# Optimization experiments

Hardware: AMD Instinct MI355X
Metric: run time of the kernel (lower is better)

## Reference

```python
import jax, jax.numpy as jnp
import numpy as np

B, S, I, E, D = 64, 512, 64, 256, 256  # batch, src_len, input_size, enc_hid, dec_hid


def _lstm_cell(h, c, x, Wih, Whh, b):
    # PyTorch LSTM gate order: i, f, g, o ; b = b_ih + b_hh combined
    z = x @ Wih.T + h @ Whh.T + b
    i, f, g, o = jnp.split(z, 4, axis=-1)
    c = jax.nn.sigmoid(f) * c + jax.nn.sigmoid(i) * jnp.tanh(g)
    h = jax.nn.sigmoid(o) * jnp.tanh(c)
    return h, c


def _run_lstm(x, h0, c0, Wih, Whh, b):
    # x: [B,S,I] -> outputs [B,S,H]
    def step(carry, xt):
        h, c = _lstm_cell(carry[0], carry[1], xt, Wih, Whh, b)
        return (h, c), h
    _, ys = jax.lax.scan(step, (h0, c0), jnp.swapaxes(x, 0, 1))
    return jnp.swapaxes(ys, 0, 1)


def _forward(x, enc_h0, enc_c0, dec_h0, dec_c0, Wih_f, Whh_f, b_f, Wih_b, Whh_b, b_b,
             W_attn, b_attn, v, Wih_d, Whh_d, b_d, W_lin, b_lin):
    b_, s_ = x.shape[0], x.shape[1]
    # bidirectional encoder
    out_f = _run_lstm(x, enc_h0[0], enc_c0[0], Wih_f, Whh_f, b_f)
    out_b = _run_lstm(x[:, ::-1, :], enc_h0[1], enc_c0[1], Wih_b, Whh_b, b_b)[:, ::-1, :]
    enc_out = jnp.concatenate([out_f, out_b], axis=-1)  # [B,S,2E]
    h0d, c0d = dec_h0[0], dec_c0[0]  # decoder re-starts from these EVERY step (faithful)

    @jax.checkpoint
    def dec_step(carry, _):
        y, h_attn = carry  # y: [B,1], h_attn: [B,D]
        dh = h_attn.shape[-1]
        cat = jnp.concatenate(
            [jnp.broadcast_to(h_attn[:, None, :], (b_, s_, dh)), enc_out], axis=-1)
        energy = jnp.tanh(cat @ W_attn.T + b_attn)              # [B,S,D]
        attn = jax.nn.softmax(jnp.einsum('d,bsd->bs', v, energy), axis=1)
        context = jnp.einsum('bs,bse->be', attn, enc_out)       # [B,2E]
        dec_in = jnp.concatenate([y, context], axis=-1)         # [B,1+2E]
        h_new, _c = _lstm_cell(h0d, c0d, dec_in, Wih_d, Whh_d, b_d)
        y_new = jnp.concatenate([h_new, context], axis=-1) @ W_lin.T + b_lin  # [B,1]
        return (y_new, h_new), y_new

    y0 = jnp.zeros((b_, 1), dtype=x.dtype)
    _, ys = jax.lax.scan(dec_step, (y0, h0d), None, length=s_)  # [S,B,1]
    # output_size == 1, so torch's cat-then-[:,1:] equals the stacked per-step ys
    return jnp.swapaxes(ys, 0, 1).reshape(b_, s_)


def setup_inputs() -> dict:
    key = jax.random.key(0)
    ks = jax.random.split(key, 20)
    W = 0.05  # weight scale ~ torch default init magnitude
    rn = lambda k, sh, s: jax.random.normal(k, sh, dtype=jnp.float32) * s
    return {
        'x': rn(ks[0], (B, S, I), 1.0),
        'enc_h0': rn(ks[1], (2, B, E), 1.0),
        'enc_c0': rn(ks[2], (2, B, E), 1.0),
        'dec_h0': rn(ks[3], (1, B, D), 1.0),
        'dec_c0': rn(ks[4], (1, B, D), 1.0),
        'Wih_f': rn(ks[5], (4 * E, I), W),
        'Whh_f': rn(ks[6], (4 * E, E), W),
        'b_f': rn(ks[7], (4 * E,), W),
        'Wih_b': rn(ks[8], (4 * E, I), W),
        'Whh_b': rn(ks[9], (4 * E, E), W),
        'b_b': rn(ks[10], (4 * E,), W),
        'W_attn': rn(ks[11], (D, D + 2 * E), W),
        'b_attn': rn(ks[12], (D,), W),
        'v': jax.random.uniform(ks[13], (D,), dtype=jnp.float32),
        'Wih_d': rn(ks[14], (4 * D, 2 * E + 1), W),
        'Whh_d': rn(ks[15], (4 * D, D), W),
        'b_d': rn(ks[16], (4 * D,), W),
        'W_lin': rn(ks[17], (1, 2 * E + D), W),
        'b_lin': rn(ks[18], (1,), W),
    }


def reference(x, enc_h0, enc_c0, dec_h0, dec_c0, Wih_f, Whh_f, b_f, Wih_b, Whh_b, b_b,
              W_attn, b_attn, v, Wih_d, Whh_d, b_d, W_lin, b_lin):
    return _forward(x, enc_h0, enc_c0, dec_h0, dec_c0, Wih_f, Whh_f, b_f,
                    Wih_b, Whh_b, b_b, W_attn, b_attn, v, Wih_d, Whh_d, b_d,
                    W_lin, b_lin)
```

## Files before the change

kernel.cpp:

```cpp
#include <hip/hip_runtime.h>
#include <hip/hip_bf16.h>

#define NB 64
#define NS 512
#define NI 64
#define NE 256
#define ND 256
#define N4E 1024
#define N4D 1024
#define NTE 512
#define G 4
#define SLICE 128
#define CELLS 64

__device__ __forceinline__ float fsig(float x){
    return __fdividef(1.f, 1.f + __expf(-x));
}
__device__ __forceinline__ float ftanh(float x){
    return 1.f - __fdividef(2.f, 1.f + __expf(2.f*x));
}
__device__ __forceinline__ float wave_sum(float v){
    #pragma unroll
    for (int o=32;o>0;o>>=1) v += __shfl_xor(v, o, 64);
    return v;
}
__device__ __forceinline__ float wave_max(float v){
    #pragma unroll
    for (int o=32;o>0;o>>=1) v = fmaxf(v, __shfl_xor(v, o, 64));
    return v;
}
__device__ __forceinline__ float blo(unsigned u){ return __uint_as_float(u<<16); }
__device__ __forceinline__ float bhi(unsigned u){ return __uint_as_float(u & 0xffff0000u); }
__device__ __forceinline__ unsigned short bfbits(float f){
    __hip_bfloat16 h = __float2bfloat16(f);
    return *(unsigned short*)&h;
}
__device__ __forceinline__ float ld_agf(const float* p){
    return __hip_atomic_load(p, __ATOMIC_RELAXED, __HIP_MEMORY_SCOPE_AGENT);
}
__device__ __forceinline__ void st_agf(float* p, float v){
    __hip_atomic_store(p, v, __ATOMIC_RELAXED, __HIP_MEMORY_SCOPE_AGENT);
}
__device__ __forceinline__ unsigned long long ld_ag64(const unsigned long long* p){
    return __hip_atomic_load(p, __ATOMIC_RELAXED, __HIP_MEMORY_SCOPE_AGENT);
}
__device__ __forceinline__ void st_ag64(unsigned long long* p, unsigned long long v){
    __hip_atomic_store(p, v, __ATOMIC_RELAXED, __HIP_MEMORY_SCOPE_AGENT);
}

__device__ __forceinline__ void groupbar(unsigned* flags, int b, int q,
                                         unsigned tgt, int tid){
    __syncthreads();
    if (tid == 0)
        __hip_atomic_store(&flags[(b<<5)+q], tgt, __ATOMIC_RELAXED, __HIP_MEMORY_SCOPE_AGENT);
    if (tid < G){
        while (__hip_atomic_load(&flags[(b<<5)+tid], __ATOMIC_RELAXED,
                                 __HIP_MEMORY_SCOPE_AGENT) < tgt)
            ;
    }
    __syncthreads();
}

__global__ void k_transpose(float* __restrict__ dst, const float* __restrict__ src,
                            int R, int C, int ld, int off){
    int idx = blockIdx.x*256 + threadIdx.x;
    if (idx >= R*C) return;
    int r = idx / C, c = idx - r*C;
    dst[(size_t)c*R + r] = src[(size_t)r*ld + off + c];
}
__global__ void k_transpose16(__hip_bfloat16* __restrict__ dst, const float* __restrict__ src,
                              int R, int C, int ld, int off){
    int idx = blockIdx.x*256 + threadIdx.x;
    if (idx >= R*C) return;
    int r = idx / C, c = idx - r*C;
    dst[(size_t)c*R + r] = __float2bfloat16(src[(size_t)r*ld + off + c]);
}

__global__ void k_pack_wy(float* __restrict__ wy, const float* __restrict__ Wih_d){
    int j = blockIdx.x*256 + threadIdx.x;
    if (j < N4D) wy[j] = Wih_d[(size_t)j*(NTE+1)];
}

__global__ void k_pack_wdtg(__hip_bfloat16* __restrict__ dst, const float* __restrict__ Wih_d){
    int idx = blockIdx.x*256 + threadIdx.x;
    int q = idx >> 17, rem = idx & 131071;
    int e = rem >> 8, jj = rem & 255;
    int j = ((jj>>6)<<8) + (q<<6) + (jj&63);
    dst[idx] = __float2bfloat16(Wih_d[(size_t)j*(NTE+1) + 1 + e]);
}

__global__ void k_zc(float* __restrict__ zc, const float* __restrict__ WhhTd,
                     const float* __restrict__ h0d, const float* __restrict__ b_d){
    int b = blockIdx.x, tid = threadIdx.x;
    __shared__ float h0[ND];
    if (tid < ND) h0[tid] = h0d[b*ND + tid];
    __syncthreads();
    for (int j = tid; j < N4D; j += 256){
        float acc = b_d[j];
        #pragma unroll 8
        for (int d=0; d<ND; ++d) acc = fmaf(h0[d], WhhTd[d*N4D + j], acc);
        zc[b*N4D + j] = acc;
    }
}

__global__ void k_dec_init(float* __restrict__ hG, float* __restrict__ yG,
                           unsigned* __restrict__ flags, const float* __restrict__ dec_h0){
    int b = blockIdx.x, tid = threadIdx.x;
    hG[b*ND + tid] = dec_h0[b*ND + tid];
    if (tid < G){ yG[(b<<5) + tid] = 0.f; flags[(b<<5) + tid] = 0u; }
}

__global__ __launch_bounds__(1024) void k_enc(
    const float* __restrict__ x, const float* __restrict__ eh0, const float* __restrict__ ec0,
    const unsigned* __restrict__ whhTf, const unsigned* __restrict__ wihTf, const float* __restrict__ bf,
    const unsigned* __restrict__ whhTb, const unsigned* __restrict__ wihTb, const float* __restrict__ bb,
    unsigned* __restrict__ eo32)
{
    int bid = blockIdx.x;
    int b = bid & 63, dir = bid >> 6;
    int tid = threadIdx.x;
    int j2 = tid & 511, kh = tid >> 9;
    const unsigned* whh = dir ? whhTb : whhTf;
    const unsigned* wih = dir ? wihTb : wihTf;
    const float* bias = dir ? bb : bf;

    __shared__ __align__(16) float h_l[NE];
    __shared__ __align__(16) float xt[2][NI];
    __shared__ float zp0[N4E], zp1[N4E];

    float2 bias2 = make_float2(0.f, 0.f);
    if (kh == 0) bias2 = ((const float2*)bias)[j2];

    float cst = 0.f;
    if (tid < NE){
        h_l[tid] = eh0[(dir*NB+b)*NE + tid];
        cst      = ec0[(dir*NB+b)*NE + tid];
    }
    {
        int st0 = dir ? (NS-1) : 0;
        if (tid < 16) ((float4*)xt[0])[tid] = ((const float4*)(x + ((size_t)b*NS+st0)*NI))[tid];
    }
    __syncthreads();

    const unsigned* wihK = wih + (size_t)(kh*32)*512 + j2;
    const unsigned* whhK = whh + (size_t)(kh*128)*512 + j2;
    float* zpme = kh ? zp1 : zp0;

    for (int t=0;t<NS;++t){
        int st = dir ? (NS-1-t) : t;
        float4 xpre = make_float4(0.f,0.f,0.f,0.f);
        if (t+1 < NS && tid < 16){
            int stn = dir ? (NS-2-t) : (t+1);
            xpre = ((const float4*)(x + ((size_t)b*NS+stn)*NI))[tid];
        }
        const float* xc = xt[t&1];
        float x0=bias2.x, y0=bias2.y, x1=0.f, y1=0.f;
        #pragma unroll 8
        for (int ii=0; ii<32; ii+=2){
            int i = kh*32 + ii;
            unsigned wa = wihK[(size_t)ii*512];
            unsigned wb = wihK[(size_t)(ii+1)*512];
            float xa = xc[i], xb = xc[i+1];
            x0 = fmaf(xa, blo(wa), x0); y0 = fmaf(xa, bhi(wa), y0);
            x1 = fmaf(xb, blo(wb), x1); y1 = fmaf(xb, bhi(wb), y1);
        }
        #pragma unroll 8
        for (int dd=0; dd<128; dd+=2){
            int d = kh*128 + dd;
            unsigned wa = whhK[(size_t)dd*512];
            unsigned wb = whhK[(size_t)(dd+1)*512];
            float ha = h_l[d], hb = h_l[d+1];
            x0 = fmaf(ha, blo(wa), x0); y0 = fmaf(ha, bhi(wa), y0);
            x1 = fmaf(hb, blo(wb), x1); y1 = fmaf(hb, bhi(wb), y1);
        }
        ((float2*)zpme)[j2] = make_float2(x0+x1, y0+y1);
        if (t+1 < NS && tid < 16) ((float4*)xt[(t+1)&1])[tid] = xpre;
        __syncthreads();
        if (tid < NE){
            int c = tid;
            float zi = zp0[c]        + zp1[c];
            float zf = zp0[NE+c]     + zp1[NE+c];
            float zg = zp0[2*NE+c]   + zp1[2*NE+c];
            float zo = zp0[3*NE+c]   + zp1[3*NE+c];
            cst = fsig(zf)*cst + fsig(zi)*ftanh(zg);
            float hn = fsig(zo)*ftanh(cst);
            h_l[c] = hn;
            ((unsigned short*)eo32)[((size_t)b*NS+st)*NTE + dir*NE + c] = bfbits(hn);
        }
        __syncthreads();
    }
}

__global__ __launch_bounds__(256) void k_encproj(const unsigned* __restrict__ eo32,
        const float* __restrict__ WeT, const float* __restrict__ b_attn,
        unsigned short* __restrict__ ep_pk16){
    int b = blockIdx.y, s0 = blockIdx.x*16, tid = threadIdx.x;
    __shared__ float tile[16*NTE];
    {
        const unsigned* eop = eo32 + (size_t)(b*NS + s0)*256;
        for (int k=0;k<32;++k){
            int wi = k*256 + tid;
            unsigned w = eop[wi];
            int sl = wi>>8, ew = wi&255;
            tile[sl*NTE + 2*ew]   = blo(w);
            tile[sl*NTE + 2*ew+1] = bhi(w);
        }
    }
    __syncthreads();
    float acc[16];
    float ba = b_attn[tid];
    #pragma unroll
    for (int sl=0;sl<16;++sl) acc[sl]=ba;
    #pragma unroll 4
    for (int e4=0;e4<128;++e4){
        float w0 = WeT[(4*e4+0)*ND+tid];
        float w1 = WeT[(4*e4+1)*ND+tid];
        float w2 = WeT[(4*e4+2)*ND+tid];
        float w3 = WeT[(4*e4+3)*ND+tid];
        #pragma unroll
        for (int sl=0;sl<16;++sl){
            const float4 tv = *(const float4*)&tile[sl*NTE + 4*e4];
            acc[sl] = fmaf(tv.x,w0,fmaf(tv.y,w1,fmaf(tv.z,w2,fmaf(tv.w,w3,acc[sl]))));
        }
    }
    #pragma unroll
    for (int sl=0;sl<16;++sl){
        int s = s0+sl;
        size_t wdi = ((size_t)(b*4 + (s>>7))*128 + (tid>>1))*128 + (s&127);
        ep_pk16[wdi*2 + (tid&1)] = bfbits(acc[sl]);
    }
}

__global__ __launch_bounds__(1024) void k_dec(
    const unsigned* __restrict__ eo32,
    const unsigned* __restrict__ ep_pk,
    const unsigned* __restrict__ WhTp,
    const float* __restrict__ v,
    const float* __restrict__ zc, const float* __restrict__ wy,
    const unsigned* __restrict__ WdTp_all,
    const float* __restrict__ dec_c0,
    const float* __restrict__ W_lin, const float* __restrict__ b_lin,
    float* __restrict__ hG, float* __restrict__ yG,
    float* __restrict__ ctxG, float* __restrict__ msG,
    unsigned* __restrict__ flags,
    float* __restrict__ out)
{
    int bid = blockIdx.x;
    int b = bid & 63, q = bid >> 6;
    int tid = threadIdx.x;
    int w = tid >> 6, l = tid & 63;

    __shared__ unsigned ep_lds[16384];
    __shared__ float part[2048];
    __shared__ float h_l[ND];
    __shared__ float2 hv[ND];
    __shared__ float scraw[SLICE];
    __shared__ float scores_p[4*33];
    __shared__ float ctx_l[NTE];
    __shared__ float z_l[256], zc_l[256], wy_l[256];
    __shared__ float c0_l[CELLS], wlh_l[CELLS], wlc_l[SLICE];
    __shared__ float msbuf[8];
    __shared__ float wred[16];
    __shared__ float yprev;

    const unsigned* WdTp = WdTp_all + (size_t)q*NTE*128;

    for (int i=tid; i<16384; i+=1024)
        ep_lds[i] = ep_pk[(size_t)(b*4+q)*16384 + i];
    unsigned eo_reg[32];
    {
        int sq = l & 3, ep2 = w*16 + (l>>2);
        const unsigned* eop = eo32 + (size_t)(b*NS + q*SLICE + sq*32)*256 + ep2;
        #pragma unroll
        for (int ss=0; ss<32; ++ss) eo_reg[ss] = eop[(size_t)ss*256];
    }
    if (tid < 256){
        int jj = tid;
        int j = ((jj>>6)<<8) + (q<<6) + (jj&63);
        zc_l[jj] = zc[b*N4D + j];
        wy_l[jj] = wy[j];
    }
    if (tid < ND) hv[tid] = make_float2(v[tid], 0.f);
    if (tid < CELLS){
        c0_l[tid]  = dec_c0[b*ND + q*CELLS + tid];
        wlh_l[tid] = W_lin[q*CELLS + tid];
    }
    if (tid < SLICE) wlc_l[tid] = W_lin[ND + q*SLICE + tid];
    float blin = b_lin[0];
    __syncthreads();

    for (int t=0; t<NS; ++t){
        if (tid < 128){
            unsigned long long hh = ld_ag64((const unsigned long long*)(hG + b*ND) + tid);
            float2 h2 = *(float2*)&hh;
            h_l[2*tid]   = h2.x;
            h_l[2*tid+1] = h2.y;
        }
        __syncthreads();
        {
            int d2 = tid & 127, kq = tid >> 7;
            float ax = 0.f, ay = 0.f;
            #pragma unroll 8
            for (int kk=0; kk<32; ++kk){
                int k = kq*32 + kk;
                unsigned ww = WhTp[k*128 + d2];
                float hvv = h_l[k];
                ax = fmaf(hvv, blo(ww), ax); ay = fmaf(hvv, bhi(ww), ay);
            }
            ((float2*)part)[kq*128 + d2] = make_float2(ax, ay);
        }
        __syncthreads();
        if (tid < ND)
            hv[tid].y = part[tid] + part[256+tid] + part[512+tid] + part[768+tid]
                      + part[1024+tid] + part[1280+tid] + part[1536+tid] + part[1792+tid];
        __syncthreads();
        {
            int sl = tid & 127, dg = tid >> 7;
            float sc = 0.f;
            const unsigned* epl = ep_lds + dg*16*128 + sl;
            #pragma unroll
            for (int k16=0; k16<16; ++k16){
                unsigned ww = epl[k16*128];
                int d = dg*32 + 2*k16;
                float2 a0 = hv[d], a1 = hv[d+1];
                sc += a0.x*ftanh(blo(ww) + a0.y) + a1.x*ftanh(bhi(ww) + a1.y);
            }
            part[dg*128 + sl] = sc;
        }
        __syncthreads();
        if (tid < SLICE){
            float s = 0.f;
            #pragma unroll
            for (int r=0;r<8;++r) s += part[r*128 + tid];
            scraw[tid] = s;
            float wm = wave_max(s);
            if ((tid&63)==0) wred[tid>>6] = wm;
        }
        __syncthreads();
        float smax = fmaxf(wred[0], wred[1]);
        if (tid < SLICE){
            float ev = __expf(scraw[tid] - smax);
            scores_p[(tid>>5)*33 + (tid&31)] = ev;
            float s = wave_sum(ev);
            if ((tid&63)==0) wred[2+(tid>>6)] = s;
        }
        __syncthreads();
        if (tid == 0){
            st_agf(&msG[(b<<5) + 2*q + 0], smax);
            st_agf(&msG[(b<<5) + 2*q + 1], wred[2]+wred[3]);
        }
        {
            int sq = l & 3, ep2 = w*16 + (l>>2);
            float ax = 0.f, ay = 0.f;
            const float* sp = scores_p + sq*33;
            #pragma unroll
            for (int ss=0; ss<32; ++ss){
                float p = sp[ss];
                unsigned e = eo_reg[ss];
                ax = fmaf(p, blo(e), ax); ay = fmaf(p, bhi(e), ay);
            }
            ax += __shfl_xor(ax, 1, 64); ay += __shfl_xor(ay, 1, 64);
            ax += __shfl_xor(ax, 2, 64); ay += __shfl_xor(ay, 2, 64);
            if (sq == 0) ((float2*)part)[ep2] = make_float2(ax, ay);
        }
        __syncthreads();
        if (tid < 256){
            float2 c2 = ((float2*)part)[tid];
            st_ag64((unsigned long long*)(ctxG + (size_t)(b*4+q)*NTE + 2*tid),
                    *(unsigned long long*)&c2);
        }
        groupbar(flags, b, q, (unsigned)(2*t+1), tid);
        if (tid == 0){
            float y = 0.f;
            if (t > 0){
                y = blin + ld_agf(&yG[(b<<5)+0]) + ld_agf(&yG[(b<<5)+1])
                         + ld_agf(&yG[(b<<5)+2]) + ld_agf(&yG[(b<<5)+3]);
                if (q == 0) out[(size_t)b*NS + (t-1)] = y;
            }
            yprev = y;
        }
        unsigned long long cg[4];
        if (tid < 8) msbuf[tid] = ld_agf(&msG[(b<<5) + tid]);
        if (tid < 256){
            const unsigned long long* cgp =
                (const unsigned long long*)(ctxG + (size_t)b*4*NTE) + tid;
            #pragma unroll
            for (int qq=0; qq<4; ++qq) cg[qq] = ld_ag64(cgp + qq*256);
        }
        __syncthreads();
        if (tid < 256){
            float mm = fmaxf(fmaxf(msbuf[0], msbuf[2]), fmaxf(msbuf[4], msbuf[6]));
            float w0 = __expf(msbuf[0]-mm), w1 = __expf(msbuf[2]-mm),
                  w2 = __expf(msbuf[4]-mm), w3 = __expf(msbuf[6]-mm);
            float inv = __fdividef(1.f, msbuf[1]*w0 + msbuf[3]*w1 + msbuf[5]*w2 + msbuf[7]*w3);
            float2 c0v = *(float2*)&cg[0], c1v = *(float2*)&cg[1];
            float2 c2v = *(float2*)&cg[2], c3v = *(float2*)&cg[3];
            float ax = c0v.x*w0 + c1v.x*w1 + c2v.x*w2 + c3v.x*w3;
            float ay = c0v.y*w0 + c1v.y*w1 + c2v.y*w2 + c3v.y*w3;
            ((float2*)ctx_l)[tid] = make_float2(ax*inv, ay*inv);
        }
        __syncthreads();
        {
            int jj2 = tid & 127, eq = tid >> 7;
            float ax = 0.f, ay = 0.f;
            #pragma unroll 8
            for (int ee=0; ee<64; ++ee){
                int e = eq*64 + ee;
                unsigned ww = WdTp[e*128 + jj2];
                float cv = ctx_l[e];
                ax = fmaf(cv, blo(ww), ax); ay = fmaf(cv, bhi(ww), ay);
            }
            ((float2*)part)[eq*128 + jj2] = make_float2(ax, ay);
        }
        __syncthreads();
        if (tid < 256){
            float s = zc_l[tid] + yprev*wy_l[tid];
            #pragma unroll
            for (int r=0; r<8; ++r) s += part[r*256 + tid];
            z_l[tid] = s;
        }
        __syncthreads();
        float yp = 0.f;
        if (tid < CELLS){
            float zi=z_l[tid], zf=z_l[64+tid], zg=z_l[128+tid], zo=z_l[192+tid];
            float cn = fsig(zf)*c0_l[tid] + fsig(zi)*ftanh(zg);
            float hn = fsig(zo)*ftanh(cn);
            st_agf(&hG[b*ND + q*CELLS + tid], hn);
            yp = hn * wlh_l[tid];
        } else if (tid < CELLS + SLICE){
            yp = ctx_l[q*SLICE + (tid - CELLS)] * wlc_l[tid - CELLS];
        }
        {
            float s = wave_sum(yp);
            if ((tid&63)==0 && tid < 192) wred[8+(tid>>6)] = s;
        }
        __syncthreads();
        if (tid == 0) st_agf(&yG[(b<<5) + q], wred[8]+wred[9]+wred[10]);
        groupbar(flags, b, q, (unsigned)(2*t+2), tid);
    }
    if (q == 0 && tid == 0){
        out[(size_t)b*NS + (NS-1)] = blin + ld_agf(&yG[(b<<5)+0]) + ld_agf(&yG[(b<<5)+1])
                                          + ld_agf(&yG[(b<<5)+2]) + ld_agf(&yG[(b<<5)+3]);
    }
}

extern "C" void kernel_launch(void* const* d_in, const int* in_sizes, int n_in,
                              void* d_out, int out_size, void* d_ws, size_t ws_size,
                              hipStream_t stream){
    const float* x      = (const float*)d_in[0];
    const float* enc_h0 = (const float*)d_in[1];
    const float* enc_c0 = (const float*)d_in[2];
    const float* dec_h0 = (const float*)d_in[3];
    const float* dec_c0 = (const float*)d_in[4];
    const float* Wih_f  = (const float*)d_in[5];
    const float* Whh_f  = (const float*)d_in[6];
    const float* b_f    = (const float*)d_in[7];
    const float* Wih_b  = (const float*)d_in[8];
    const float* Whh_b  = (const float*)d_in[9];
    const float* b_b    = (const float*)d_in[10];
    const float* W_attn = (const float*)d_in[11];
    const float* b_attn = (const float*)d_in[12];
    const float* v      = (const float*)d_in[13];
    const float* Wih_d  = (const float*)d_in[14];
    const float* Whh_d  = (const float*)d_in[15];
    const float* b_d    = (const float*)d_in[16];
    const float* W_lin  = (const float*)d_in[17];
    const float* b_lin  = (const float*)d_in[18];
    float* out = (float*)d_out;
    char* ws   = (char*)d_ws;

    size_t off = 0;
    auto alloc = [&](size_t bytes)->size_t{ size_t o = off; off += (bytes + 255) & ~(size_t)255; return o; };
    size_t o_eo16   = alloc((size_t)NB*NS*NTE*2);
    size_t o_eppk   = alloc((size_t)NB*G*128*128*4);
    size_t o_WihTf  = alloc((size_t)NI*N4E*2);
    size_t o_WhhTf  = alloc((size_t)NE*N4E*2);
    size_t o_WihTb  = alloc((size_t)NI*N4E*2);
    size_t o_WhhTb  = alloc((size_t)NE*N4E*2);
    size_t o_WhT16  = alloc((size_t)ND*ND*2);
    size_t o_WeT    = alloc((size_t)NTE*ND*4);
    size_t o_WdTg   = alloc((size_t)G*NTE*256*2);
    size_t o_WhhTd  = alloc((size_t)ND*N4D*4);
    size_t o_zc     = alloc((size_t)NB*N4D*4);
    size_t o_wy     = alloc((size_t)N4D*4);
    size_t o_hG     = alloc((size_t)NB*ND*4);
    size_t o_yG     = alloc((size_t)NB*32*4);
    size_t o_ctxG   = alloc((size_t)NB*G*NTE*4);
    size_t o_msG    = alloc((size_t)NB*32*4);
    size_t o_flags  = alloc((size_t)NB*32*4);
    if (ws_size < off) return;

    auto F   = [&](size_t o)->float*{ return (float*)(ws + o); };
    auto U32 = [&](size_t o)->unsigned*{ return (unsigned*)(ws + o); };
    auto H16 = [&](size_t o)->__hip_bfloat16*{ return (__hip_bfloat16*)(ws + o); };

    auto T32 = [&](size_t dsto, const float* src, int R, int C, int ld, int offc){
        int n = R*C;
        k_transpose<<<dim3((n+255)/256), dim3(256), 0, stream>>>(F(dsto), src, R, C, ld, offc);
    };
    auto T16 = [&](size_t dsto, const float* src, int R, int C, int ld, int offc){
        int n = R*C;
        k_transpose16<<<dim3((n+255)/256), dim3(256), 0, stream>>>(H16(dsto), src, R, C, ld, offc);
    };
    T16(o_WihTf, Wih_f, N4E, NI, NI, 0);
    T16(o_WhhTf, Whh_f, N4E, NE, NE, 0);
    T16(o_WihTb, Wih_b, N4E, NI, NI, 0);
    T16(o_WhhTb, Whh_b, N4E, NE, NE, 0);
    T16(o_WhT16, W_attn, ND, ND, ND+NTE, 0);
    T32(o_WeT,   W_attn, ND, NTE, ND+NTE, ND);
    T32(o_WhhTd, Whh_d, N4D, ND, ND, 0);
    k_pack_wdtg<<<dim3((G*NTE*256)/256), dim3(256), 0, stream>>>(H16(o_WdTg), Wih_d);
    k_pack_wy<<<dim3(4), dim3(256), 0, stream>>>(F(o_wy), Wih_d);
    k_zc<<<dim3(NB), dim3(256), 0, stream>>>(F(o_zc), F(o_WhhTd), dec_h0, b_d);
    k_dec_init<<<dim3(NB), dim3(256), 0, stream>>>(F(o_hG), F(o_yG), (unsigned*)(ws+o_flags), dec_h0);

    k_enc<<<dim3(2*NB), dim3(1024), 0, stream>>>(x, enc_h0, enc_c0,
        U32(o_WhhTf), U32(o_WihTf), b_f, U32(o_WhhTb), U32(o_WihTb), b_b, U32(o_eo16));

    k_encproj<<<dim3(NS/16, NB), dim3(256), 0, stream>>>(U32(o_eo16), F(o_WeT), b_attn,
        (unsigned short*)(ws+o_eppk));

    k_dec<<<dim3(NB*G), dim3(1024), 0, stream>>>(U32(o_eo16), U32(o_eppk),
        U32(o_WhT16), v, F(o_zc), F(o_wy), U32(o_WdTg), dec_c0, W_lin, b_lin,
        F(o_hG), F(o_yG), F(o_ctxG), F(o_msG), (unsigned*)(ws+o_flags), out);
}
```

Before: 18.40 ms.

## Compute full decoder LSTM cell redundantly per block to drop a grid barrier

Each of the four cooperating blocks per batch row now computes all 1024 decoder gates and the whole LSTM cell locally, instead of computing a quarter and exchanging h and y through global memory. This removes the second per-timestep group barrier and the global h/y round trips. The price is four times the Wih_d context matvec per block, reading the full packed bf16 weight matrix each step, plus more LDS.

Result: faster. 18.03 ms (-2.0%).

```diff
diff --git a/kernel.cpp b/kernel.cpp
--- a/kernel.cpp
+++ b/kernel.cpp
@@ -11,7 +11,6 @@
 #define NTE 512
 #define G 4
 #define SLICE 128
-#define CELLS 64
 
 __device__ __forceinline__ float fsig(float x){
     return __fdividef(1.f, 1.f + __expf(-x));
@@ -81,12 +80,12 @@
     if (j < N4D) wy[j] = Wih_d[(size_t)j*(NTE+1)];
 }
 
-__global__ void k_pack_wdtg(__hip_bfloat16* __restrict__ dst, const float* __restrict__ Wih_d){
+__global__ void k_pack_wdtf(unsigned* __restrict__ dst, const float* __restrict__ Wih_d){
     int idx = blockIdx.x*256 + threadIdx.x;
-    int q = idx >> 17, rem = idx & 131071;
-    int e = rem >> 8, jj = rem & 255;
-    int j = ((jj>>6)<<8) + (q<<6) + (jj&63);
-    dst[idx] = __float2bfloat16(Wih_d[(size_t)j*(NTE+1) + 1 + e]);
+    int e = idx >> 9, j2 = idx & 511;
+    unsigned lo = bfbits(Wih_d[(size_t)(2*j2)*(NTE+1) + 1 + e]);
+    unsigned hi = bfbits(Wih_d[(size_t)(2*j2+1)*(NTE+1) + 1 + e]);
+    dst[idx] = lo | (hi<<16);
 }
 
 __global__ void k_zc(float* __restrict__ zc, const float* __restrict__ WhhTd,
@@ -103,11 +102,9 @@
     }
 }
 
-__global__ void k_dec_init(float* __restrict__ hG, float* __restrict__ yG,
-                           unsigned* __restrict__ flags, const float* __restrict__ dec_h0){
+__global__ void k_dec_init(unsigned* __restrict__ flags){
     int b = blockIdx.x, tid = threadIdx.x;
-    hG[b*ND + tid] = dec_h0[b*ND + tid];
-    if (tid < G){ yG[(b<<5) + tid] = 0.f; flags[(b<<5) + tid] = 0u; }
+    if (tid < G) flags[(b<<5) + tid] = 0u;
 }
 
 __global__ __launch_bounds__(1024) void k_enc(
@@ -237,10 +234,9 @@
     const unsigned* __restrict__ WhTp,
     const float* __restrict__ v,
     const float* __restrict__ zc, const float* __restrict__ wy,
-    const unsigned* __restrict__ WdTp_all,
-    const float* __restrict__ dec_c0,
+    const uint2* __restrict__ wdT2,
+    const float* __restrict__ dec_h0, const float* __restrict__ dec_c0,
     const float* __restrict__ W_lin, const float* __restrict__ b_lin,
-    float* __restrict__ hG, float* __restrict__ yG,
     float* __restrict__ ctxG, float* __restrict__ msG,
     unsigned* __restrict__ flags,
     float* __restrict__ out)
@@ -251,19 +247,17 @@
     int w = tid >> 6, l = tid & 63;
 
     __shared__ unsigned ep_lds[16384];
-    __shared__ float part[2048];
+    __shared__ float part[4096];
     __shared__ float h_l[ND];
     __shared__ float2 hv[ND];
     __shared__ float scraw[SLICE];
     __shared__ float scores_p[4*33];
     __shared__ float ctx_l[NTE];
-    __shared__ float z_l[256], zc_l[256], wy_l[256];
-    __shared__ float c0_l[CELLS], wlh_l[CELLS], wlc_l[SLICE];
+    __shared__ float z_l[N4D], zc_l[N4D], wy_l[N4D];
+    __shared__ float c0_l[ND], wlh_l[ND], wlc_l[NTE];
     __shared__ float msbuf[8];
     __shared__ float wred[16];
     __shared__ float yprev;
-
-    const unsigned* WdTp = WdTp_all + (size_t)q*NTE*128;
 
     for (int i=tid; i<16384; i+=1024)
         ep_lds[i] = ep_pk[(size_t)(b*4+q)*16384 + i];
@@ -274,29 +268,20 @@
         #pragma unroll
         for (int ss=0; ss<32; ++ss) eo_reg[ss] = eop[(size_t)ss*256];
     }
-    if (tid < 256){
-        int jj = tid;
-        int j = ((jj>>6)<<8) + (q<<6) + (jj&63);
-        zc_l[jj] = zc[b*N4D + j];
-        wy_l[jj] = wy[j];
-    }
-    if (tid < ND) hv[tid] = make_float2(v[tid], 0.f);
-    if (tid < CELLS){
-        c0_l[tid]  = dec_c0[b*ND + q*CELLS + tid];
-        wlh_l[tid] = W_lin[q*CELLS + tid];
-    }
-    if (tid < SLICE) wlc_l[tid] = W_lin[ND + q*SLICE + tid];
+    zc_l[tid] = zc[b*N4D + tid];
+    wy_l[tid] = wy[tid];
+    if (tid < ND){
+        hv[tid]    = make_float2(v[tid], 0.f);
+        h_l[tid]   = dec_h0[b*ND + tid];
+        c0_l[tid]  = dec_c0[b*ND + tid];
+        wlh_l[tid] = W_lin[tid];
+    }
+    if (tid < NTE) wlc_l[tid] = W_lin[ND + tid];
+    if (tid == 0) yprev = 0.f;
     float blin = b_lin[0];
     __syncthreads();
 
     for (int t=0; t<NS; ++t){
-        if (tid < 128){
-            unsigned long long hh = ld_ag64((const unsigned long long*)(hG + b*ND) + tid);
-            float2 h2 = *(float2*)&hh;
-            h_l[2*tid]   = h2.x;
-            h_l[2*tid+1] = h2.y;
-        }
-        __syncthreads();
         {
             int d2 = tid & 127, kq = tid >> 7;
             float ax = 0.f, ay = 0.f;
@@ -369,16 +354,7 @@
             st_ag64((unsigned long long*)(ctxG + (size_t)(b*4+q)*NTE + 2*tid),
                     *(unsigned long long*)&c2);
         }
-        groupbar(flags, b, q, (unsigned)(2*t+1), tid);
-        if (tid == 0){
-            float y = 0.f;
-            if (t > 0){
-                y = blin + ld_agf(&yG[(b<<5)+0]) + ld_agf(&yG[(b<<5)+1])
-                         + ld_agf(&yG[(b<<5)+2]) + ld_agf(&yG[(b<<5)+3]);
-                if (q == 0) out[(size_t)b*NS + (t-1)] = y;
-            }
-            yprev = y;
-        }
+        groupbar(flags, b, q, (unsigned)(t+1), tid);
         unsigned long long cg[4];
         if (tid < 8) msbuf[tid] = ld_agf(&msG[(b<<5) + tid]);
         if (tid < 256){
@@ -401,46 +377,45 @@
         }
         __syncthreads();
         {
-            int jj2 = tid & 127, eq = tid >> 7;
-            float ax = 0.f, ay = 0.f;
+            int p4 = tid & 255, eq = tid >> 8;
+            float a0=0.f, a1=0.f, a2=0.f, a3=0.f;
+            const uint2* wp = wdT2 + (size_t)(eq*128)*256 + p4;
             #pragma unroll 8
-            for (int ee=0; ee<64; ++ee){
-                int e = eq*64 + ee;
-                unsigned ww = WdTp[e*128 + jj2];
-                float cv = ctx_l[e];
-                ax = fmaf(cv, blo(ww), ax); ay = fmaf(cv, bhi(ww), ay);
+            for (int ee=0; ee<128; ++ee){
+                uint2 ww = wp[(size_t)ee*256];
+                float cv = ctx_l[eq*128 + ee];
+                a0 = fmaf(cv, blo(ww.x), a0); a1 = fmaf(cv, bhi(ww.x), a1);
+                a2 = fmaf(cv, blo(ww.y), a2); a3 = fmaf(cv, bhi(ww.y), a3);
             }
-            ((float2*)part)[eq*128 + jj2] = make_float2(ax, ay);
-        }
-        __syncthreads();
-        if (tid < 256){
-            float s = zc_l[tid] + yprev*wy_l[tid];
-            #pragma unroll
-            for (int r=0; r<8; ++r) s += part[r*256 + tid];
-            z_l[tid] = s;
-        }
+            ((float4*)part)[eq*256 + p4] = make_float4(a0,a1,a2,a3);
+        }
+        __syncthreads();
+        z_l[tid] = zc_l[tid] + yprev*wy_l[tid]
+                 + part[tid] + part[1024+tid] + part[2048+tid] + part[3072+tid];
         __syncthreads();
         float yp = 0.f;
-        if (tid < CELLS){
-            float zi=z_l[tid], zf=z_l[64+tid], zg=z_l[128+tid], zo=z_l[192+tid];
+        if (tid < ND){
+            float zi=z_l[tid], zf=z_l[ND+tid], zg=z_l[2*ND+tid], zo=z_l[3*ND+tid];
             float cn = fsig(zf)*c0_l[tid] + fsig(zi)*ftanh(zg);
             float hn = fsig(zo)*ftanh(cn);
-            st_agf(&hG[b*ND + q*CELLS + tid], hn);
+            h_l[tid] = hn;
             yp = hn * wlh_l[tid];
-        } else if (tid < CELLS + SLICE){
-            yp = ctx_l[q*SLICE + (tid - CELLS)] * wlc_l[tid - CELLS];
+        } else if (tid < ND + NTE){
+            yp = ctx_l[tid - ND] * wlc_l[tid - ND];
         }
         {
             float s = wave_sum(yp);
-            if ((tid&63)==0 && tid < 192) wred[8+(tid>>6)] = s;
-        }
-        __syncthreads();
-        if (tid == 0) st_agf(&yG[(b<<5) + q], wred[8]+wred[9]+wred[10]);
-        groupbar(flags, b, q, (unsigned)(2*t+2), tid);
-    }
-    if (q == 0 && tid == 0){
-        out[(size_t)b*NS + (NS-1)] = blin + ld_agf(&yG[(b<<5)+0]) + ld_agf(&yG[(b<<5)+1])
-                                          + ld_agf(&yG[(b<<5)+2]) + ld_agf(&yG[(b<<5)+3]);
+            if ((tid&63)==0 && tid < 768) wred[tid>>6] = s;
+        }
+        __syncthreads();
+        if (tid == 0){
+            float y = blin;
+            #pragma unroll
+            for (int g=0; g<12; ++g) y += wred[g];
+            if (q == 0) out[(size_t)b*NS + t] = y;
+            yprev = y;
+        }
+        __syncthreads();
     }
 }
 
@@ -479,12 +454,10 @@
     size_t o_WhhTb  = alloc((size_t)NE*N4E*2);
     size_t o_WhT16  = alloc((size_t)ND*ND*2);
     size_t o_WeT    = alloc((size_t)NTE*ND*4);
-    size_t o_WdTg   = alloc((size_t)G*NTE*256*2);
+    size_t o_Wdtf   = alloc((size_t)NTE*512*4);
     size_t o_WhhTd  = alloc((size_t)ND*N4D*4);
     size_t o_zc     = alloc((size_t)NB*N4D*4);
     size_t o_wy     = alloc((size_t)N4D*4);
-    size_t o_hG     = alloc((size_t)NB*ND*4);
-    size_t o_yG     = alloc((size_t)NB*32*4);
     size_t o_ctxG   = alloc((size_t)NB*G*NTE*4);
     size_t o_msG    = alloc((size_t)NB*32*4);
     size_t o_flags  = alloc((size_t)NB*32*4);
@@ -509,10 +482,10 @@
     T16(o_WhT16, W_attn, ND, ND, ND+NTE, 0);
     T32(o_WeT,   W_attn, ND, NTE, ND+NTE, ND);
     T32(o_WhhTd, Whh_d, N4D, ND, ND, 0);
-    k_pack_wdtg<<<dim3((G*NTE*256)/256), dim3(256), 0, stream>>>(H16(o_WdTg), Wih_d);
+    k_pack_wdtf<<<dim3((NTE*512)/256), dim3(256), 0, stream>>>(U32(o_Wdtf), Wih_d);
     k_pack_wy<<<dim3(4), dim3(256), 0, stream>>>(F(o_wy), Wih_d);
     k_zc<<<dim3(NB), dim3(256), 0, stream>>>(F(o_zc), F(o_WhhTd), dec_h0, b_d);
-    k_dec_init<<<dim3(NB), dim3(256), 0, stream>>>(F(o_hG), F(o_yG), (unsigned*)(ws+o_flags), dec_h0);
+    k_dec_init<<<dim3(NB), dim3(64), 0, stream>>>((unsigned*)(ws+o_flags));
 
     k_enc<<<dim3(2*NB), dim3(1024), 0, stream>>>(x, enc_h0, enc_c0,
         U32(o_WhhTf), U32(o_WihTf), b_f, U32(o_WhhTb), U32(o_WihTb), b_b, U32(o_eo16));
@@ -521,6 +494,7 @@
         (unsigned short*)(ws+o_eppk));
 
     k_dec<<<dim3(NB*G), dim3(1024), 0, stream>>>(U32(o_eo16), U32(o_eppk),
-        U32(o_WhT16), v, F(o_zc), F(o_wy), U32(o_WdTg), dec_c0, W_lin, b_lin,
-        F(o_hG), F(o_yG), F(o_ctxG), F(o_msG), (unsigned*)(ws+o_flags), out);
-}
+        U32(o_WhT16), v, F(o_zc), F(o_wy), (const uint2*)(ws+o_Wdtf),
+        dec_h0, dec_c0, W_lin, b_lin,
+        F(o_ctxG), F(o_msG), (unsigned*)(ws+o_flags), out);
+}
```
